# Optimization experiments

Hardware: AMD Instinct MI355X
Metric: run time of the kernel (lower is better)

Reference implementation:

```python
import jax, jax.numpy as jnp
import numpy as np

VEC = 64
HEADS = 16
DUP = 4
HIDDEN = VEC * HEADS * DUP  # 4096
EPS = 1e-12


def setup_inputs() -> dict:
    key = jax.random.key(0)
    ks = jax.random.split(key, 7)
    B, S, N = 4, 512, 512
    out_len = VEC * HEADS
    return {
        "embeddings": jax.random.normal(ks[0], (B, S, HIDDEN), jnp.float32),
        "keys": jax.random.normal(ks[1], (B, N, out_len), jnp.float32),
        "values": jax.random.normal(ks[2], (B, N, out_len), jnp.float32),
        "Wq": jax.random.normal(ks[3], (HIDDEN, HIDDEN), jnp.float32) * (1.0 / np.sqrt(HIDDEN)),
        "bq": jnp.zeros((HIDDEN,), jnp.float32),
        "Wre": jax.random.normal(ks[4], (HIDDEN, HIDDEN), jnp.float32) * (1.0 / np.sqrt(HIDDEN)),
        "bre": jnp.zeros((HIDDEN,), jnp.float32),
        "ln_g": jnp.ones((HIDDEN,), jnp.float32),
        "ln_b": jnp.zeros((HIDDEN,), jnp.float32),
    }


def reference(embeddings, keys, values, Wq, bq, Wre, bre, ln_g, ln_b):
    B, S, _ = embeddings.shape
    N = keys.shape[1]
    # query projection: (B,S,hidden) -> reshape to (B, S*DUP, VEC, HEADS) -> (B,H,S*DUP,VEC)
    q = embeddings @ Wq.T + bq
    q = q.reshape(B, S * DUP, VEC, HEADS).transpose(0, 3, 1, 2)
    # keys: (B,N,VEC*HEADS) -> (B,H,VEC,N); values -> (B,H,N,VEC)
    k = keys.reshape(B, N, VEC, HEADS).transpose(0, 3, 2, 1)
    v = values.reshape(B, N, VEC, HEADS).transpose(0, 3, 1, 2)
    scores = jnp.matmul(q, k) / np.sqrt(VEC).astype(np.float32)  # (B,H,S*DUP,N)
    probs = jax.nn.softmax(scores, axis=-1)
    out = jnp.matmul(probs, v)  # (B,H,S*DUP,VEC)
    # (B,H,S*DUP,VEC) -> (B,H,S,VEC*DUP) -> (B,S,H,VEC*DUP) -> (B,S,HIDDEN)
    out = out.reshape(B, HEADS, S, VEC * DUP).transpose(0, 2, 1, 3).reshape(B, S, HIDDEN)
    # LayerNorm (biased variance, torch semantics)
    mu = jnp.mean(out, axis=-1, keepdims=True)
    var = jnp.mean(jnp.square(out - mu), axis=-1, keepdims=True)
    ln = (out - mu) / jnp.sqrt(var + EPS) * ln_g + ln_b
    return ln @ Wre.T + bre
```

## Files before the change

### kernel.cpp

```cpp
#include <hip/hip_runtime.h>

typedef __attribute__((ext_vector_type(8))) _Float16 half8;
typedef __attribute__((ext_vector_type(4))) _Float16 half4;
typedef __attribute__((ext_vector_type(4))) float    floatx4;

#define GLD16(g, l)                                                            \
  __builtin_amdgcn_global_load_lds(                                            \
      (const __attribute__((address_space(1))) void*)(g),                      \
      (__attribute__((address_space(3))) void*)(l), 16, 0, 0)

__device__ __forceinline__ void cvt8(const float* __restrict__ in,
                                     _Float16* __restrict__ out, int i) {
  const float4* p = (const float4*)in + (size_t)i * 2;
  float4 a = p[0], b = p[1];
  half8 h;
  h[0] = (_Float16)a.x; h[1] = (_Float16)a.y; h[2] = (_Float16)a.z; h[3] = (_Float16)a.w;
  h[4] = (_Float16)b.x; h[5] = (_Float16)b.y; h[6] = (_Float16)b.z; h[7] = (_Float16)b.w;
  *(half8*)(out + (size_t)i * 8) = h;
}

__global__ __launch_bounds__(256) void prepA(const float* __restrict__ emb,
                                             const float* __restrict__ Wq,
                                             const float* __restrict__ keys,
                                             const float* __restrict__ values,
                                             _Float16* __restrict__ embH,
                                             _Float16* __restrict__ WqH,
                                             _Float16* __restrict__ Kh,
                                             _Float16* __restrict__ Vt) {
  const int bid = blockIdx.x, t = threadIdx.x;
  if (bid < 4096) {
    cvt8(emb, embH, bid * 256 + t);
  } else if (bid < 12288) {
    cvt8(Wq, WqH, (bid - 4096) * 256 + t);
  } else {
    const int tid = (bid - 12288) * 256 + t;
    {
      int v = tid & 63, n = (tid >> 6) & 511, h = (tid >> 15) & 15, b = tid >> 19;
      Kh[tid] = (_Float16)keys[((size_t)(b * 512 + n)) * 1024 + v * 16 + h];
    }
    {
      int n = tid & 511, v = (tid >> 9) & 63, h = (tid >> 15) & 15, b = tid >> 19;
      Vt[tid] = (_Float16)values[((size_t)(b * 512 + n)) * 1024 + v * 16 + h];
    }
  }
}

template <int MODE>
__global__ __launch_bounds__(256, 3) void gemm_bt(const _Float16* __restrict__ A,
                                                  const _Float16* __restrict__ Bw,
                                                  const float* __restrict__ bias,
                                                  float* __restrict__ Cf,
                                                  _Float16* __restrict__ H0,
                                                  _Float16* __restrict__ H1) {
  const int K = 4096;
  __shared__ _Float16 lA[128 * 64];
  __shared__ _Float16 lB[128 * 64];
  const int t = threadIdx.x, lane = t & 63, w = t >> 6;
  const int m0 = blockIdx.y * 128, n0 = blockIdx.x * 128;
  const int kb = blockIdx.z * 2048;
  const int wm = (w >> 1) * 64, wn = (w & 1) * 64;
  const int fr = lane & 15, fq = lane >> 4;

  floatx4 acc[4][4];
#pragma unroll
  for (int i = 0; i < 4; i++)
#pragma unroll
    for (int j = 0; j < 4; j++) acc[i][j] = (floatx4)(0.f);

  const int srow = t >> 3;
  const int sch = (t & 7) ^ (srow & 7);
  const _Float16* gA = A + (size_t)(m0 + srow) * K + kb + sch * 8;
  const _Float16* gB = Bw + (size_t)(n0 + srow) * K + kb + sch * 8;
  _Float16* dA = &lA[t * 8];
  _Float16* dB = &lB[t * 8];

  for (int k0 = 0; k0 < 2048; k0 += 64) {
    GLD16(gA, dA);
    GLD16(gA + (size_t)32 * K, dA + 2048);
    GLD16(gA + (size_t)64 * K, dA + 4096);
    GLD16(gA + (size_t)96 * K, dA + 6144);
    GLD16(gB, dB);
    GLD16(gB + (size_t)32 * K, dB + 2048);
    GLD16(gB + (size_t)64 * K, dB + 4096);
    GLD16(gB + (size_t)96 * K, dB + 6144);
    gA += 64;
    gB += 64;
    __syncthreads();
#pragma unroll
    for (int ks = 0; ks < 2; ks++) {
      half8 af[4], bf[4];
#pragma unroll
      for (int i = 0; i < 4; i++) {
        const int rr = wm + i * 16 + fr;
        af[i] = *(const half8*)&lA[rr * 64 + (((ks * 4 + fq) ^ (rr & 7)) * 8)];
      }
#pragma unroll
      for (int j = 0; j < 4; j++) {
        const int rr = wn + j * 16 + fr;
        bf[j] = *(const half8*)&lB[rr * 64 + (((ks * 4 + fq) ^ (rr & 7)) * 8)];
      }
#pragma unroll
      for (int i = 0; i < 4; i++)
#pragma unroll
        for (int j = 0; j < 4; j++)
          acc[i][j] =
              __builtin_amdgcn_mfma_f32_16x16x32_f16(af[i], bf[j], acc[i][j], 0, 0, 0);
    }
    __syncthreads();
  }

  const int z = blockIdx.z;
#pragma unroll
  for (int i = 0; i < 4; i++)
#pragma unroll
    for (int j = 0; j < 4; j++) {
      const int col = n0 + wn + j * 16 + fr;
      const int rbase = m0 + wm + i * 16 + fq * 4;
      if (MODE == 0 && z == 0) {
        const float bv = bias[col];
#pragma unroll
        for (int r = 0; r < 4; r++)
          Cf[(size_t)(rbase + r) * 4096 + col] = acc[i][j][r] + bv;
      } else {
        _Float16* P = z ? H1 : H0;
#pragma unroll
        for (int r = 0; r < 4; r++)
          P[(size_t)(rbase + r) * 4096 + col] = (_Float16)acc[i][j][r];
      }
    }
}

__global__ __launch_bounds__(256) void prepB(const float* __restrict__ Wre,
                                             _Float16* __restrict__ WreH,
                                             const _Float16* __restrict__ p0,
                                             const _Float16* __restrict__ p1,
                                             const float* __restrict__ bq,
                                             _Float16* __restrict__ q) {
  const int bid = blockIdx.x, t = threadIdx.x;
  if (bid < 8192) {
    cvt8(Wre, WreH, bid * 256 + t);
    return;
  }
  __shared__ _Float16 T[4][16][80];
  const int L = t & 63, w = t >> 6;
  const int m = bid - 8192, d = w;
  const int b = m >> 9, s = m & 511;
  const size_t src = (size_t)m * 4096 + d * 1024 + L * 16;
  half8 a0 = *(const half8*)(p0 + src);
  half8 a1 = *(const half8*)(p0 + src + 8);
  half8 b0 = *(const half8*)(p1 + src);
  half8 b1 = *(const half8*)(p1 + src + 8);
  const float4* bqv = (const float4*)(bq + d * 1024 + L * 16);
  float bias[16];
#pragma unroll
  for (int c = 0; c < 4; c++) {
    float4 f = bqv[c];
    bias[c * 4 + 0] = f.x; bias[c * 4 + 1] = f.y;
    bias[c * 4 + 2] = f.z; bias[c * 4 + 3] = f.w;
  }
#pragma unroll
  for (int h = 0; h < 8; h++) {
    T[w][h][L] = (_Float16)(((float)a0[h] + (float)b0[h] + bias[h]) * 0.125f);
    T[w][h + 8][L] =
        (_Float16)(((float)a1[h] + (float)b1[h] + bias[h + 8]) * 0.125f);
  }
  const int h2 = L >> 2, c2 = L & 3;
  _Float16* dst = q + (((size_t)(b * 16 + h2) * 2048) + s * 4 + d) * 64 + c2 * 8;
  *(half8*)dst = *(const half8*)&T[w][h2][c2 * 8];
  *(half8*)(dst + 32) = *(const half8*)&T[w][h2][32 + c2 * 8];
}

__global__ __launch_bounds__(256) void combine2(float* __restrict__ out,
                                                const _Float16* __restrict__ p1) {
  const int i4 = (blockIdx.x * 256 + threadIdx.x) * 4;
  float4 o = *(float4*)&out[i4];
  half4 p = *(const half4*)(p1 + i4);
  o.x += (float)p[0];
  o.y += (float)p[1];
  o.z += (float)p[2];
  o.w += (float)p[3];
  *(float4*)&out[i4] = o;
}

__global__ __launch_bounds__(256) void attn_mfma(const _Float16* __restrict__ Q,
                                                 const _Float16* __restrict__ Kh,
                                                 const _Float16* __restrict__ Vt,
                                                 float* __restrict__ Out) {
  __shared__ _Float16 Pbuf[4][32][136];
  const int t = threadIdx.x, lane = t & 63, w = t >> 6;
  const int fr = lane & 15, fq = lane >> 4;
  const int bh = blockIdx.y, qt = blockIdx.x;
  const int b = bh >> 4, h = bh & 15;

  const _Float16* Qb = Q + ((size_t)bh * 2048 + qt * 128 + w * 32) * 64;
  const _Float16* Kb = Kh + (size_t)bh * 512 * 64;
  const _Float16* Vb = Vt + (size_t)bh * 64 * 512;

  half8 qf[2][2];
#pragma unroll
  for (int i = 0; i < 2; i++)
#pragma unroll
    for (int ks = 0; ks < 2; ks++)
      qf[i][ks] = *(const half8*)(Qb + (i * 16 + fr) * 64 + ks * 32 + fq * 8);

  floatx4 oacc[2][4];
  float l_acc[2][4];
#pragma unroll
  for (int i = 0; i < 2; i++)
#pragma unroll
    for (int j = 0; j < 4; j++) {
      oacc[i][j] = (floatx4)(0.f);
      l_acc[i][j] = 0.f;
    }

  for (int c0 = 0; c0 < 512; c0 += 128) {
    floatx4 sc[2][8];
#pragma unroll
    for (int i = 0; i < 2; i++)
#pragma unroll
      for (int j = 0; j < 8; j++) sc[i][j] = (floatx4)(0.f);
#pragma unroll
    for (int j = 0; j < 8; j++) {
      const _Float16* kr = Kb + (size_t)(c0 + j * 16 + fr) * 64 + fq * 8;
      half8 k0 = *(const half8*)kr;
      half8 k1 = *(const half8*)(kr + 32);
#pragma unroll
      for (int i = 0; i < 2; i++) {
        sc[i][j] = __builtin_amdgcn_mfma_f32_16x16x32_f16(qf[i][0], k0, sc[i][j], 0, 0, 0);
        sc[i][j] = __builtin_amdgcn_mfma_f32_16x16x32_f16(qf[i][1], k1, sc[i][j], 0, 0, 0);
      }
    }
#pragma unroll
    for (int i = 0; i < 2; i++)
#pragma unroll
      for (int j = 0; j < 8; j++)
#pragma unroll
        for (int r = 0; r < 4; r++) {
          float p = __expf(sc[i][j][r]);
          l_acc[i][r] += p;
          Pbuf[w][i * 16 + fq * 4 + r][j * 16 + fr] = (_Float16)p;
        }
#pragma unroll
    for (int kn = 0; kn < 4; kn++) {
      half8 pa[2];
#pragma unroll
      for (int i = 0; i < 2; i++)
        pa[i] = *(const half8*)&Pbuf[w][i * 16 + fr][kn * 32 + fq * 8];
#pragma unroll
      for (int jv = 0; jv < 4; jv++) {
        half8 vb = *(const half8*)(Vb + (size_t)(jv * 16 + fr) * 512 + c0 + kn * 32 + fq * 8);
#pragma unroll
        for (int i = 0; i < 2; i++)
          oacc[i][jv] = __builtin_amdgcn_mfma_f32_16x16x32_f16(pa[i], vb, oacc[i][jv], 0, 0, 0);
      }
    }
  }

#pragma unroll
  for (int i = 0; i < 2; i++)
#pragma unroll
    for (int r = 0; r < 4; r++) {
#pragma unroll
      for (int m = 8; m; m >>= 1)
        l_acc[i][r] += __shfl_xor(l_acc[i][r], m, 16);
    }
#pragma unroll
  for (int i = 0; i < 2; i++) {
#pragma unroll
    for (int r = 0; r < 4; r++) {
      const float inv = 1.f / l_acc[i][r];
      const int m2 = qt * 128 + w * 32 + i * 16 + fq * 4 + r;
      float* orow = Out + ((size_t)(b * 512 + (m2 >> 2))) * 4096 + h * 256 + (m2 & 3) * 64 + fr;
#pragma unroll
      for (int jv = 0; jv < 4; jv++) orow[jv * 16] = oacc[i][jv][r] * inv;
    }
  }
}

__global__ __launch_bounds__(256) void ln_kernel(const float* __restrict__ X,
                                                 const float* __restrict__ g,
                                                 const float* __restrict__ bb,
                                                 _Float16* __restrict__ Y) {
  const int row = blockIdx.x;
  const int t = threadIdx.x;
  const float* x = X + (size_t)row * 4096;
  float4 vals[4];
  float sum = 0.f, sq = 0.f;
#pragma unroll
  for (int c = 0; c < 4; c++) {
    vals[c] = *(const float4*)&x[c * 1024 + t * 4];
    sum += vals[c].x + vals[c].y + vals[c].z + vals[c].w;
    sq += vals[c].x * vals[c].x + vals[c].y * vals[c].y + vals[c].z * vals[c].z +
          vals[c].w * vals[c].w;
  }
#pragma unroll
  for (int off = 32; off > 0; off >>= 1) {
    sum += __shfl_down(sum, off, 64);
    sq += __shfl_down(sq, off, 64);
  }
  __shared__ float red[8];
  const int w = t >> 6;
  if ((t & 63) == 0) {
    red[w] = sum;
    red[4 + w] = sq;
  }
  __syncthreads();
  sum = red[0] + red[1] + red[2] + red[3];
  sq = red[4] + red[5] + red[6] + red[7];
  const float mu = sum * (1.f / 4096.f);
  float var = sq * (1.f / 4096.f) - mu * mu;
  var = fmaxf(var, 0.f);
  const float rstd = rsqrtf(var + 1e-12f);
#pragma unroll
  for (int c = 0; c < 4; c++) {
    const int j = c * 1024 + t * 4;
    float4 gg = *(const float4*)&g[j];
    float4 bv = *(const float4*)&bb[j];
    half4 y;
    y[0] = (_Float16)((vals[c].x - mu) * rstd * gg.x + bv.x);
    y[1] = (_Float16)((vals[c].y - mu) * rstd * gg.y + bv.y);
    y[2] = (_Float16)((vals[c].z - mu) * rstd * gg.z + bv.z);
    y[3] = (_Float16)((vals[c].w - mu) * rstd * gg.w + bv.w);
    *(half4*)&Y[(size_t)row * 4096 + j] = y;
  }
}

extern "C" void kernel_launch(void* const* d_in, const int* in_sizes, int n_in,
                              void* d_out, int out_size, void* d_ws,
                              size_t ws_size, hipStream_t stream) {
  const float* emb = (const float*)d_in[0];
  const float* keys = (const float*)d_in[1];
  const float* values = (const float*)d_in[2];
  const float* Wq = (const float*)d_in[3];
  const float* bq = (const float*)d_in[4];
  const float* Wre = (const float*)d_in[5];
  const float* bre = (const float*)d_in[6];
  const float* ln_g = (const float*)d_in[7];
  const float* ln_b = (const float*)d_in[8];
  float* out = (float*)d_out;

  char* ws = (char*)d_ws;
  _Float16* embH = (_Float16*)(ws);
  _Float16* WqH = (_Float16*)(ws + ((size_t)16 << 20));
  _Float16* Kh = (_Float16*)(ws + ((size_t)48 << 20));
  _Float16* Vt = (_Float16*)(ws + ((size_t)52 << 20));
  _Float16* P0q = (_Float16*)d_out;
  _Float16* P1q = (_Float16*)((char*)d_out + ((size_t)16 << 20));
  _Float16* WreH = WqH;
  _Float16* qattn = (_Float16*)(ws);
  _Float16* lnH = (_Float16*)(ws + ((size_t)48 << 20));
  _Float16* P1o = (_Float16*)(ws);

  prepA<<<20480, 256, 0, stream>>>(emb, Wq, keys, values, embH, WqH, Kh, Vt);
  gemm_bt<1><<<dim3(32, 16, 2), 256, 0, stream>>>(embH, WqH, nullptr, nullptr,
                                                  P0q, P1q);
  prepB<<<10240, 256, 0, stream>>>(Wre, WreH, P0q, P1q, bq, qattn);
  attn_mfma<<<dim3(16, 64), 256, 0, stream>>>(qattn, Kh, Vt, out);
  ln_kernel<<<2048, 256, 0, stream>>>(out, ln_g, ln_b, lnH);
  gemm_bt<0><<<dim3(32, 16, 2), 256, 0, stream>>>(lnH, WreH, bre, out, nullptr,
                                                  P1o);
  combine2<<<8192, 256, 0, stream>>>(out, P1o);
}
```

Baseline: 467.0 us.

## Fuse query bias/transpose into attention, emit fp16 attention output, merge LN prep

The separate prepB pass is removed. The attention kernel now gathers the two split-K query partials plus the bias directly, scales by 1/8 and builds its Q fragments in registers. Attention writes its output as fp16 instead of fp32, and LayerNorm is folded into the Wre conversion kernel (prepC), which saves one launch and roughly half of the intermediate traffic. The K/V transpose in prepA now reads coalesced float4s and handles four heads per thread. The costs are strided scalar Q loads inside attention and an extra fp16 rounding of the attention output before LayerNorm.

```diff
diff --git a/kernel.cpp b/kernel.cpp
--- a/kernel.cpp
+++ b/kernel.cpp
@@ -1,8 +1,8 @@
 #include <hip/hip_runtime.h>
 
-typedef __attribute__((ext_vector_type(8))) _Float16 half8;
-typedef __attribute__((ext_vector_type(4))) _Float16 half4;
-typedef __attribute__((ext_vector_type(4))) float    floatx4;
+typedef __attribute__((ext_vector_type(8)))  _Float16 half8;
+typedef __attribute__((ext_vector_type(4)))  _Float16 half4;
+typedef __attribute__((ext_vector_type(4)))  float    floatx4;
 
 #define GLD16(g, l)                                                            \
   __builtin_amdgcn_global_load_lds(                                            \
@@ -34,13 +34,19 @@
     cvt8(Wq, WqH, (bid - 4096) * 256 + t);
   } else {
     const int tid = (bid - 12288) * 256 + t;
-    {
-      int v = tid & 63, n = (tid >> 6) & 511, h = (tid >> 15) & 15, b = tid >> 19;
-      Kh[tid] = (_Float16)keys[((size_t)(b * 512 + n)) * 1024 + v * 16 + h];
-    }
-    {
-      int n = tid & 511, v = (tid >> 9) & 63, h = (tid >> 15) & 15, b = tid >> 19;
-      Vt[tid] = (_Float16)values[((size_t)(b * 512 + n)) * 1024 + v * 16 + h];
+    const int q4 = tid & 3, v = (tid >> 2) & 63, n = (tid >> 8) & 511,
+              b = tid >> 17;
+    const size_t src = ((size_t)(b * 512 + n)) * 256 + v * 4 + q4;
+    float4 kk = ((const float4*)keys)[src];
+    float4 vv = ((const float4*)values)[src];
+    const float* kf = (const float*)&kk;
+    const float* vf = (const float*)&vv;
+#pragma unroll
+    for (int j = 0; j < 4; j++) {
+      const int h = q4 * 4 + j;
+      const size_t bh = (size_t)(b * 16 + h);
+      Kh[(bh * 512 + n) * 64 + v] = (_Float16)kf[j];
+      Vt[(bh * 64 + v) * 512 + n] = (_Float16)vf[j];
     }
   }
 }
@@ -130,44 +136,173 @@
     }
 }
 
-__global__ __launch_bounds__(256) void prepB(const float* __restrict__ Wre,
+__global__ __launch_bounds__(256) void attn_mfma(const _Float16* __restrict__ p0,
+                                                 const _Float16* __restrict__ p1,
+                                                 const float* __restrict__ bq,
+                                                 const _Float16* __restrict__ Kh,
+                                                 const _Float16* __restrict__ Vt,
+                                                 _Float16* __restrict__ Out) {
+  __shared__ _Float16 Pbuf[4][32][136];
+  const int t = threadIdx.x, lane = t & 63, w = t >> 6;
+  const int fr = lane & 15, fq = lane >> 4;
+  const int bh = blockIdx.y, qt = blockIdx.x;
+  const int b = bh >> 4, h = bh & 15;
+
+  const _Float16* Kb = Kh + (size_t)bh * 512 * 64;
+  const _Float16* Vb = Vt + (size_t)bh * 64 * 512;
+
+  half8 qf[2][2];
+#pragma unroll
+  for (int i = 0; i < 2; i++) {
+    const int m2 = qt * 128 + w * 32 + i * 16 + fr;
+    const int s = m2 >> 2, d = m2 & 3;
+    const size_t rowb = ((size_t)(b * 512 + s)) * 4096 + d * 1024 + h;
+    const int bcol = d * 1024 + h;
+#pragma unroll
+    for (int ks = 0; ks < 2; ks++) {
+      const int v0 = ks * 32 + fq * 8;
+      const _Float16* a0 = p0 + rowb + v0 * 16;
+      const _Float16* a1 = p1 + rowb + v0 * 16;
+      const float* bb = bq + bcol + v0 * 16;
+      half8 q;
+#pragma unroll
+      for (int j = 0; j < 8; j++)
+        q[j] = (_Float16)(((float)a0[j * 16] + (float)a1[j * 16] + bb[j * 16]) *
+                          0.125f);
+      qf[i][ks] = q;
+    }
+  }
+
+  floatx4 oacc[2][4];
+  float l_acc[2][4];
+#pragma unroll
+  for (int i = 0; i < 2; i++)
+#pragma unroll
+    for (int j = 0; j < 4; j++) {
+      oacc[i][j] = (floatx4)(0.f);
+      l_acc[i][j] = 0.f;
+    }
+
+  for (int c0 = 0; c0 < 512; c0 += 128) {
+    floatx4 sc[2][8];
+#pragma unroll
+    for (int i = 0; i < 2; i++)
+#pragma unroll
+      for (int j = 0; j < 8; j++) sc[i][j] = (floatx4)(0.f);
+#pragma unroll
+    for (int j = 0; j < 8; j++) {
+      const _Float16* kr = Kb + (size_t)(c0 + j * 16 + fr) * 64 + fq * 8;
+      half8 k0 = *(const half8*)kr;
+      half8 k1 = *(const half8*)(kr + 32);
+#pragma unroll
+      for (int i = 0; i < 2; i++) {
+        sc[i][j] = __builtin_amdgcn_mfma_f32_16x16x32_f16(qf[i][0], k0, sc[i][j], 0, 0, 0);
+        sc[i][j] = __builtin_amdgcn_mfma_f32_16x16x32_f16(qf[i][1], k1, sc[i][j], 0, 0, 0);
+      }
+    }
+#pragma unroll
+    for (int i = 0; i < 2; i++)
+#pragma unroll
+      for (int j = 0; j < 8; j++)
+#pragma unroll
+        for (int r = 0; r < 4; r++) {
+          float p = __expf(sc[i][j][r]);
+          l_acc[i][r] += p;
+          Pbuf[w][i * 16 + fq * 4 + r][j * 16 + fr] = (_Float16)p;
+        }
+#pragma unroll
+    for (int kn = 0; kn < 4; kn++) {
+      half8 pa[2];
+#pragma unroll
+      for (int i = 0; i < 2; i++)
+        pa[i] = *(const half8*)&Pbuf[w][i * 16 + fr][kn * 32 + fq * 8];
+#pragma unroll
+      for (int jv = 0; jv < 4; jv++) {
+        half8 vb = *(const half8*)(Vb + (size_t)(jv * 16 + fr) * 512 + c0 + kn * 32 + fq * 8);
+#pragma unroll
+        for (int i = 0; i < 2; i++)
+          oacc[i][jv] = __builtin_amdgcn_mfma_f32_16x16x32_f16(pa[i], vb, oacc[i][jv], 0, 0, 0);
+      }
+    }
+  }
+
+#pragma unroll
+  for (int i = 0; i < 2; i++)
+#pragma unroll
+    for (int r = 0; r < 4; r++) {
+#pragma unroll
+      for (int m = 8; m; m >>= 1)
+        l_acc[i][r] += __shfl_xor(l_acc[i][r], m, 16);
+    }
+#pragma unroll
+  for (int i = 0; i < 2; i++) {
+#pragma unroll
+    for (int r = 0; r < 4; r++) {
+      const float inv = 1.f / l_acc[i][r];
+      const int m2 = qt * 128 + w * 32 + i * 16 + fq * 4 + r;
+      _Float16* orow =
+          Out + ((size_t)(b * 512 + (m2 >> 2))) * 4096 + h * 256 + (m2 & 3) * 64 + fr;
+#pragma unroll
+      for (int jv = 0; jv < 4; jv++)
+        orow[jv * 16] = (_Float16)(oacc[i][jv][r] * inv);
+    }
+  }
+}
+
+__global__ __launch_bounds__(256) void prepC(const float* __restrict__ Wre,
                                              _Float16* __restrict__ WreH,
-                                             const _Float16* __restrict__ p0,
-                                             const _Float16* __restrict__ p1,
-                                             const float* __restrict__ bq,
-                                             _Float16* __restrict__ q) {
+                                             const _Float16* __restrict__ X,
+                                             const float* __restrict__ g,
+                                             const float* __restrict__ bb,
+                                             _Float16* __restrict__ Y) {
   const int bid = blockIdx.x, t = threadIdx.x;
   if (bid < 8192) {
     cvt8(Wre, WreH, bid * 256 + t);
     return;
   }
-  __shared__ _Float16 T[4][16][80];
-  const int L = t & 63, w = t >> 6;
-  const int m = bid - 8192, d = w;
-  const int b = m >> 9, s = m & 511;
-  const size_t src = (size_t)m * 4096 + d * 1024 + L * 16;
-  half8 a0 = *(const half8*)(p0 + src);
-  half8 a1 = *(const half8*)(p0 + src + 8);
-  half8 b0 = *(const half8*)(p1 + src);
-  half8 b1 = *(const half8*)(p1 + src + 8);
-  const float4* bqv = (const float4*)(bq + d * 1024 + L * 16);
-  float bias[16];
+  const int row = bid - 8192;
+  const _Float16* x = X + (size_t)row * 4096;
+  float4 vals[4];
+  float sum = 0.f, sq = 0.f;
 #pragma unroll
   for (int c = 0; c < 4; c++) {
-    float4 f = bqv[c];
-    bias[c * 4 + 0] = f.x; bias[c * 4 + 1] = f.y;
-    bias[c * 4 + 2] = f.z; bias[c * 4 + 3] = f.w;
-  }
-#pragma unroll
-  for (int h = 0; h < 8; h++) {
-    T[w][h][L] = (_Float16)(((float)a0[h] + (float)b0[h] + bias[h]) * 0.125f);
-    T[w][h + 8][L] =
-        (_Float16)(((float)a1[h] + (float)b1[h] + bias[h + 8]) * 0.125f);
-  }
-  const int h2 = L >> 2, c2 = L & 3;
-  _Float16* dst = q + (((size_t)(b * 16 + h2) * 2048) + s * 4 + d) * 64 + c2 * 8;
-  *(half8*)dst = *(const half8*)&T[w][h2][c2 * 8];
-  *(half8*)(dst + 32) = *(const half8*)&T[w][h2][32 + c2 * 8];
+    half4 hv = *(const half4*)&x[c * 1024 + t * 4];
+    vals[c].x = (float)hv[0]; vals[c].y = (float)hv[1];
+    vals[c].z = (float)hv[2]; vals[c].w = (float)hv[3];
+    sum += vals[c].x + vals[c].y + vals[c].z + vals[c].w;
+    sq += vals[c].x * vals[c].x + vals[c].y * vals[c].y + vals[c].z * vals[c].z +
+          vals[c].w * vals[c].w;
+  }
+#pragma unroll
+  for (int off = 32; off > 0; off >>= 1) {
+    sum += __shfl_down(sum, off, 64);
+    sq += __shfl_down(sq, off, 64);
+  }
+  __shared__ float red[8];
+  const int w = t >> 6;
+  if ((t & 63) == 0) {
+    red[w] = sum;
+    red[4 + w] = sq;
+  }
+  __syncthreads();
+  sum = red[0] + red[1] + red[2] + red[3];
+  sq = red[4] + red[5] + red[6] + red[7];
+  const float mu = sum * (1.f / 4096.f);
+  float var = sq * (1.f / 4096.f) - mu * mu;
+  var = fmaxf(var, 0.f);
+  const float rstd = rsqrtf(var + 1e-12f);
+#pragma unroll
+  for (int c = 0; c < 4; c++) {
+    const int j = c * 1024 + t * 4;
+    float4 gg = *(const float4*)&g[j];
+    float4 bv = *(const float4*)&bb[j];
+    half4 y;
+    y[0] = (_Float16)((vals[c].x - mu) * rstd * gg.x + bv.x);
+    y[1] = (_Float16)((vals[c].y - mu) * rstd * gg.y + bv.y);
+    y[2] = (_Float16)((vals[c].z - mu) * rstd * gg.z + bv.z);
+    y[3] = (_Float16)((vals[c].w - mu) * rstd * gg.w + bv.w);
+    *(half4*)&Y[(size_t)row * 4096 + j] = y;
+  }
 }
 
 __global__ __launch_bounds__(256) void combine2(float* __restrict__ out,
@@ -180,149 +315,6 @@
   o.z += (float)p[2];
   o.w += (float)p[3];
   *(float4*)&out[i4] = o;
-}
-
-__global__ __launch_bounds__(256) void attn_mfma(const _Float16* __restrict__ Q,
-                                                 const _Float16* __restrict__ Kh,
-                                                 const _Float16* __restrict__ Vt,
-                                                 float* __restrict__ Out) {
-  __shared__ _Float16 Pbuf[4][32][136];
-  const int t = threadIdx.x, lane = t & 63, w = t >> 6;
-  const int fr = lane & 15, fq = lane >> 4;
-  const int bh = blockIdx.y, qt = blockIdx.x;
-  const int b = bh >> 4, h = bh & 15;
-
-  const _Float16* Qb = Q + ((size_t)bh * 2048 + qt * 128 + w * 32) * 64;
-  const _Float16* Kb = Kh + (size_t)bh * 512 * 64;
-  const _Float16* Vb = Vt + (size_t)bh * 64 * 512;
-
-  half8 qf[2][2];
-#pragma unroll
-  for (int i = 0; i < 2; i++)
-#pragma unroll
-    for (int ks = 0; ks < 2; ks++)
-      qf[i][ks] = *(const half8*)(Qb + (i * 16 + fr) * 64 + ks * 32 + fq * 8);
-
-  floatx4 oacc[2][4];
-  float l_acc[2][4];
-#pragma unroll
-  for (int i = 0; i < 2; i++)
-#pragma unroll
-    for (int j = 0; j < 4; j++) {
-      oacc[i][j] = (floatx4)(0.f);
-      l_acc[i][j] = 0.f;
-    }
-
-  for (int c0 = 0; c0 < 512; c0 += 128) {
-    floatx4 sc[2][8];
-#pragma unroll
-    for (int i = 0; i < 2; i++)
-#pragma unroll
-      for (int j = 0; j < 8; j++) sc[i][j] = (floatx4)(0.f);
-#pragma unroll
-    for (int j = 0; j < 8; j++) {
-      const _Float16* kr = Kb + (size_t)(c0 + j * 16 + fr) * 64 + fq * 8;
-      half8 k0 = *(const half8*)kr;
-      half8 k1 = *(const half8*)(kr + 32);
-#pragma unroll
-      for (int i = 0; i < 2; i++) {
-        sc[i][j] = __builtin_amdgcn_mfma_f32_16x16x32_f16(qf[i][0], k0, sc[i][j], 0, 0, 0);
-        sc[i][j] = __builtin_amdgcn_mfma_f32_16x16x32_f16(qf[i][1], k1, sc[i][j], 0, 0, 0);
-      }
-    }
-#pragma unroll
-    for (int i = 0; i < 2; i++)
-#pragma unroll
-      for (int j = 0; j < 8; j++)
-#pragma unroll
-        for (int r = 0; r < 4; r++) {
-          float p = __expf(sc[i][j][r]);
-          l_acc[i][r] += p;
-          Pbuf[w][i * 16 + fq * 4 + r][j * 16 + fr] = (_Float16)p;
-        }
-#pragma unroll
-    for (int kn = 0; kn < 4; kn++) {
-      half8 pa[2];
-#pragma unroll
-      for (int i = 0; i < 2; i++)
-        pa[i] = *(const half8*)&Pbuf[w][i * 16 + fr][kn * 32 + fq * 8];
-#pragma unroll
-      for (int jv = 0; jv < 4; jv++) {
-        half8 vb = *(const half8*)(Vb + (size_t)(jv * 16 + fr) * 512 + c0 + kn * 32 + fq * 8);
-#pragma unroll
-        for (int i = 0; i < 2; i++)
-          oacc[i][jv] = __builtin_amdgcn_mfma_f32_16x16x32_f16(pa[i], vb, oacc[i][jv], 0, 0, 0);
-      }
-    }
-  }
-
-#pragma unroll
-  for (int i = 0; i < 2; i++)
-#pragma unroll
-    for (int r = 0; r < 4; r++) {
-#pragma unroll
-      for (int m = 8; m; m >>= 1)
-        l_acc[i][r] += __shfl_xor(l_acc[i][r], m, 16);
-    }
-#pragma unroll
-  for (int i = 0; i < 2; i++) {
-#pragma unroll
-    for (int r = 0; r < 4; r++) {
-      const float inv = 1.f / l_acc[i][r];
-      const int m2 = qt * 128 + w * 32 + i * 16 + fq * 4 + r;
-      float* orow = Out + ((size_t)(b * 512 + (m2 >> 2))) * 4096 + h * 256 + (m2 & 3) * 64 + fr;
-#pragma unroll
-      for (int jv = 0; jv < 4; jv++) orow[jv * 16] = oacc[i][jv][r] * inv;
-    }
-  }
-}
-
-__global__ __launch_bounds__(256) void ln_kernel(const float* __restrict__ X,
-                                                 const float* __restrict__ g,
-                                                 const float* __restrict__ bb,
-                                                 _Float16* __restrict__ Y) {
-  const int row = blockIdx.x;
-  const int t = threadIdx.x;
-  const float* x = X + (size_t)row * 4096;
-  float4 vals[4];
-  float sum = 0.f, sq = 0.f;
-#pragma unroll
-  for (int c = 0; c < 4; c++) {
-    vals[c] = *(const float4*)&x[c * 1024 + t * 4];
-    sum += vals[c].x + vals[c].y + vals[c].z + vals[c].w;
-    sq += vals[c].x * vals[c].x + vals[c].y * vals[c].y + vals[c].z * vals[c].z +
-          vals[c].w * vals[c].w;
-  }
-#pragma unroll
-  for (int off = 32; off > 0; off >>= 1) {
-    sum += __shfl_down(sum, off, 64);
-    sq += __shfl_down(sq, off, 64);
-  }
-  __shared__ float red[8];
-  const int w = t >> 6;
-  if ((t & 63) == 0) {
-    red[w] = sum;
-    red[4 + w] = sq;
-  }
-  __syncthreads();
-  sum = red[0] + red[1] + red[2] + red[3];
-  sq = red[4] + red[5] + red[6] + red[7];
-  const float mu = sum * (1.f / 4096.f);
-  float var = sq * (1.f / 4096.f) - mu * mu;
-  var = fmaxf(var, 0.f);
-  const float rstd = rsqrtf(var + 1e-12f);
-#pragma unroll
-  for (int c = 0; c < 4; c++) {
-    const int j = c * 1024 + t * 4;
-    float4 gg = *(const float4*)&g[j];
-    float4 bv = *(const float4*)&bb[j];
-    half4 y;
-    y[0] = (_Float16)((vals[c].x - mu) * rstd * gg.x + bv.x);
-    y[1] = (_Float16)((vals[c].y - mu) * rstd * gg.y + bv.y);
-    y[2] = (_Float16)((vals[c].z - mu) * rstd * gg.z + bv.z);
-    y[3] = (_Float16)((vals[c].w - mu) * rstd * gg.w + bv.w);
-    *(half4*)&Y[(size_t)row * 4096 + j] = y;
-  }
 }
 
 extern "C" void kernel_launch(void* const* d_in, const int* in_sizes, int n_in,
@@ -346,17 +338,16 @@
   _Float16* Vt = (_Float16*)(ws + ((size_t)52 << 20));
   _Float16* P0q = (_Float16*)d_out;
   _Float16* P1q = (_Float16*)((char*)d_out + ((size_t)16 << 20));
+  _Float16* attnH = (_Float16*)(ws);
   _Float16* WreH = WqH;
-  _Float16* qattn = (_Float16*)(ws);
   _Float16* lnH = (_Float16*)(ws + ((size_t)48 << 20));
   _Float16* P1o = (_Float16*)(ws);
 
-  prepA<<<20480, 256, 0, stream>>>(emb, Wq, keys, values, embH, WqH, Kh, Vt);
+  prepA<<<14336, 256, 0, stream>>>(emb, Wq, keys, values, embH, WqH, Kh, Vt);
   gemm_bt<1><<<dim3(32, 16, 2), 256, 0, stream>>>(embH, WqH, nullptr, nullptr,
                                                   P0q, P1q);
-  prepB<<<10240, 256, 0, stream>>>(Wre, WreH, P0q, P1q, bq, qattn);
-  attn_mfma<<<dim3(16, 64), 256, 0, stream>>>(qattn, Kh, Vt, out);
-  ln_kernel<<<2048, 256, 0, stream>>>(out, ln_g, ln_b, lnH);
+  attn_mfma<<<dim3(16, 64), 256, 0, stream>>>(P0q, P1q, bq, Kh, Vt, attnH);
+  prepC<<<10240, 256, 0, stream>>>(Wre, WreH, attnH, ln_g, ln_b, lnH);
   gemm_bt<0><<<dim3(32, 16, 2), 256, 0, stream>>>(lnH, WreH, bre, out, nullptr,
                                                   P1o);
   combine2<<<8192, 256, 0, stream>>>(out, P1o);
```

New measurement: 510.5 us. +9.3%, slower.
